# Kernel tuning notes

Measured on AMD Instinct MI355X. Metric: run time of the kernel, lower is better.

## Reference

```python
import jax, jax.numpy as jnp
import numpy as np
from jax import lax

NUM_STATES = 16
NUM_CHAINS = 2
NUM_NODES = 2000
NUM_ITERS = 1000


def setup_inputs() -> dict:
    key = jax.random.key(0)
    k0, k1, k2, k3 = jax.random.split(key, 4)
    return {
        "unnormalized_state_init": jax.random.normal(k0, (NUM_STATES,), dtype=jnp.float32),
        "unnormalized_chain_weights": jax.random.normal(k1, (NUM_STATES, NUM_CHAINS), dtype=jnp.float32),
        "unnormalized_emission_matrix": jax.random.normal(k2, (NUM_STATES, NUM_NODES), dtype=jnp.float32),
        "unnormalized_transition_matrix": jax.random.normal(k3, (NUM_STATES, NUM_STATES), dtype=jnp.float32),
    }


def reference(unnormalized_state_init, unnormalized_chain_weights,
              unnormalized_emission_matrix, unnormalized_transition_matrix):
    # Normalize parameters in log domain (matches torch log_softmax dims)
    log_state_init = jax.nn.log_softmax(unnormalized_state_init, axis=0)            # (S,)
    log_chain_weights = jax.nn.log_softmax(unnormalized_chain_weights, axis=1)      # (S,C)
    log_emission_matrix = jax.nn.log_softmax(unnormalized_emission_matrix, axis=1)  # (S,N)
    log_transition_matrix = jax.nn.log_softmax(unnormalized_transition_matrix, axis=1)  # (S,S)

    # Sequential HMM forward recursion in log domain:
    # h_t[j] = logsumexp_i( h_{t-1}[i] + log_T[i, j] )
    def step(h, _):
        h_next = jax.nn.logsumexp(h[:, None] + log_transition_matrix, axis=0)
        return h_next, h_next

    _, hs = lax.scan(step, log_state_init, None, length=NUM_ITERS - 1)
    log_hidden_state_probs = jnp.concatenate([log_state_init[None, :], hs], axis=0)  # (T,S)

    # P(node | state, chain, iter) joint in log domain: (T,S,C,N)
    # (original repeats emission across the 2 chains; here broadcast over C)
    log_observed_state_probs_ = (
        log_emission_matrix[None, :, None, :]
        + log_chain_weights[None, :, :, None]
        + log_hidden_state_probs[:, :, None, None]
    )
    # Marginalize states then chains (logsumexp over axes 1 then 1 == axes (1,2))
    log_observed_state_probs = jax.nn.logsumexp(log_observed_state_probs_, axis=(1, 2))  # (T,N)
    return log_observed_state_probs
```

## Files before the change

### kernel.cpp

```cpp
#include <hip/hip_runtime.h>
#include <math.h>

#define NN 2000
#define NG 500

__global__ __launch_bounds__(256) void ssm_fused(
    const float* __restrict__ init,
    const float* __restrict__ emis,
    const float* __restrict__ trans,
    float* __restrict__ out)
{
  __shared__ float Tp[16][16];
  __shared__ float Bm[16][16];
  __shared__ float Rm[16][16];
  __shared__ float p0v[16];
  __shared__ float sumExp[16];
  __shared__ float w[4][16];
  __shared__ float wd[4][16];

  const int tid  = threadIdx.x;
  const int i    = tid >> 4, j = tid & 15;
  const int lane = tid & 63, wv = tid >> 6;

  Bm[i][j] = trans[tid];

  float ssum[4] = {0.f, 0.f, 0.f, 0.f};
  for (int g = lane; g < NG; g += 64) {
    #pragma unroll
    for (int si = 0; si < 4; ++si) {
      const int s = wv * 4 + si;
      float4 v = *(const float4*)(emis + s * NN + g * 4);
      ssum[si] += __expf(v.x) + __expf(v.y) + __expf(v.z) + __expf(v.w);
    }
  }
  #pragma unroll
  for (int si = 0; si < 4; ++si) {
    float v = ssum[si];
    #pragma unroll
    for (int off = 32; off > 0; off >>= 1) v += __shfl_down(v, off);
    if (lane == 0) sumExp[wv * 4 + si] = v;
  }

  if (tid < 16) {
    float m = -1e30f, s2 = 0.f;
    #pragma unroll
    for (int k = 0; k < 16; ++k) m = fmaxf(m, init[k]);
    #pragma unroll
    for (int k = 0; k < 16; ++k) s2 += __expf(init[k] - m);
    p0v[tid] = __expf(init[tid] - m) / s2;
  }
  __syncthreads();

  {
    float m = -1e30f;
    #pragma unroll
    for (int k = 0; k < 16; ++k) m = fmaxf(m, Bm[i][k]);
    float sm = 0.f;
    #pragma unroll
    for (int k = 0; k < 16; ++k) sm += __expf(Bm[i][k] - m);
    const float tp = __expf(Bm[i][j] - m) / sm;
    __syncthreads();
    Tp[i][j] = tp;
    Bm[i][j] = tp;
    Rm[i][j] = (i == j) ? 1.f : 0.f;
  }
  __syncthreads();

  #pragma unroll
  for (int q = 0; q < 2; ++q) {
    float acc = 0.f;
    #pragma unroll
    for (int k = 0; k < 16; ++k) acc += Bm[i][k] * Bm[k][j];
    __syncthreads();
    Bm[i][j] = acc;
    __syncthreads();
  }

  int e = blockIdx.x;
  while (e) {
    const bool mul = (e & 1);
    float accR = 0.f, accB = 0.f;
    if (mul) {
      #pragma unroll
      for (int k = 0; k < 16; ++k) accR += Rm[i][k] * Bm[k][j];
    }
    #pragma unroll
    for (int k = 0; k < 16; ++k) accB += Bm[i][k] * Bm[k][j];
    __syncthreads();
    if (mul) Rm[i][j] = accR;
    Bm[i][j] = accB;
    __syncthreads();
    e >>= 1;
  }

  if (tid < 16) {
    float acc = 0.f;
    #pragma unroll
    for (int k = 0; k < 16; ++k) acc += p0v[k] * Rm[k][tid];
    w[0][tid] = acc;
  }
  __syncthreads();
  for (int tt = 1; tt < 4; ++tt) {
    if (tid < 16) {
      float acc = 0.f;
      #pragma unroll
      for (int k = 0; k < 16; ++k) acc += w[tt - 1][k] * Tp[k][tid];
      w[tt][tid] = acc;
    }
    __syncthreads();
  }
  if (tid < 64) wd[tid >> 4][tid & 15] = w[tid >> 4][tid & 15] / sumExp[tid & 15];
  __syncthreads();

  const int tbase = blockIdx.x * 4;
  for (int g = tid; g < NG; g += 256) {
    float4 ex[16];
    #pragma unroll
    for (int s = 0; s < 16; ++s) {
      float4 v = *(const float4*)(emis + s * NN + g * 4);
      ex[s].x = __expf(v.x); ex[s].y = __expf(v.y);
      ex[s].z = __expf(v.z); ex[s].w = __expf(v.w);
    }
    #pragma unroll
    for (int tt = 0; tt < 4; ++tt) {
      float4 acc = make_float4(0.f, 0.f, 0.f, 0.f);
      #pragma unroll
      for (int s = 0; s < 16; ++s) {
        const float p = wd[tt][s];
        acc.x += p * ex[s].x; acc.y += p * ex[s].y;
        acc.z += p * ex[s].z; acc.w += p * ex[s].w;
      }
      float4 o;
      o.x = __logf(acc.x); o.y = __logf(acc.y);
      o.z = __logf(acc.z); o.w = __logf(acc.w);
      *(float4*)(out + (tbase + tt) * NN + g * 4) = o;
    }
  }
}

extern "C" void kernel_launch(void* const* d_in, const int* in_sizes, int n_in,
                              void* d_out, int out_size, void* d_ws, size_t ws_size,
                              hipStream_t stream) {
  const float* init  = (const float*)d_in[0];
  const float* emis  = (const float*)d_in[2];
  const float* trans = (const float*)d_in[3];
  float* out = (float*)d_out;

  hipLaunchKernelGGL(ssm_fused, dim3(250), dim3(256), 0, stream,
                     init, emis, trans, out);
}
```

Measured before the change: 72.92 us.

## Split node columns across a 2D grid and double-buffer matrix powers

The grid becomes 2x250: each block handles 256 of the 500 float4 node groups for its four time steps, where before one block looped over all 500. The matrix-power loop now ping-pongs between two shared buffers, which removes one barrier per squaring. The identity multiply on the first set bit is skipped. Each block still redoes the emission normalisation and matrix exponentiation, so that setup work is duplicated and the second x-block is only partly used.

```diff
diff --git a/kernel.cpp b/kernel.cpp
--- a/kernel.cpp
+++ b/kernel.cpp
@@ -2,7 +2,6 @@
 #include <math.h>
 
 #define NN 2000
-#define NG 500
 
 __global__ __launch_bounds__(256) void ssm_fused(
     const float* __restrict__ init,
@@ -11,21 +10,29 @@
     float* __restrict__ out)
 {
   __shared__ float Tp[16][16];
-  __shared__ float Bm[16][16];
-  __shared__ float Rm[16][16];
+  __shared__ float Bb[2][16][16];
+  __shared__ float Rb[2][16][16];
+  __shared__ float Z[16];
+  __shared__ float wrow[4][16];
   __shared__ float p0v[16];
-  __shared__ float sumExp[16];
-  __shared__ float w[4][16];
-  __shared__ float wd[4][16];
 
   const int tid  = threadIdx.x;
   const int i    = tid >> 4, j = tid & 15;
   const int lane = tid & 63, wv = tid >> 6;
 
-  Bm[i][j] = trans[tid];
+  Rb[0][i][j] = trans[tid];
+
+  if (tid < 16) {
+    float m = -1e30f, s2 = 0.f;
+    #pragma unroll
+    for (int k = 0; k < 16; ++k) m = fmaxf(m, init[k]);
+    #pragma unroll
+    for (int k = 0; k < 16; ++k) s2 += __expf(init[k] - m);
+    p0v[tid] = __expf(init[tid] - m) / s2;
+  }
 
   float ssum[4] = {0.f, 0.f, 0.f, 0.f};
-  for (int g = lane; g < NG; g += 64) {
+  for (int g = lane; g < 500; g += 64) {
     #pragma unroll
     for (int si = 0; si < 4; ++si) {
       const int s = wv * 4 + si;
@@ -38,82 +45,84 @@
     float v = ssum[si];
     #pragma unroll
     for (int off = 32; off > 0; off >>= 1) v += __shfl_down(v, off);
-    if (lane == 0) sumExp[wv * 4 + si] = v;
-  }
-
-  if (tid < 16) {
-    float m = -1e30f, s2 = 0.f;
-    #pragma unroll
-    for (int k = 0; k < 16; ++k) m = fmaxf(m, init[k]);
-    #pragma unroll
-    for (int k = 0; k < 16; ++k) s2 += __expf(init[k] - m);
-    p0v[tid] = __expf(init[tid] - m) / s2;
+    if (lane == 0) Z[wv * 4 + si] = v;
   }
   __syncthreads();
 
   {
     float m = -1e30f;
     #pragma unroll
-    for (int k = 0; k < 16; ++k) m = fmaxf(m, Bm[i][k]);
+    for (int k = 0; k < 16; ++k) m = fmaxf(m, Rb[0][i][k]);
     float sm = 0.f;
     #pragma unroll
-    for (int k = 0; k < 16; ++k) sm += __expf(Bm[i][k] - m);
-    const float tp = __expf(Bm[i][j] - m) / sm;
+    for (int k = 0; k < 16; ++k) sm += __expf(Rb[0][i][k] - m);
+    const float tp = __expf(Rb[0][i][j] - m) / sm;
     __syncthreads();
     Tp[i][j] = tp;
-    Bm[i][j] = tp;
-    Rm[i][j] = (i == j) ? 1.f : 0.f;
+    Bb[0][i][j] = tp;
   }
   __syncthreads();
 
+  int bs = 0;
   #pragma unroll
   for (int q = 0; q < 2; ++q) {
     float acc = 0.f;
     #pragma unroll
-    for (int k = 0; k < 16; ++k) acc += Bm[i][k] * Bm[k][j];
+    for (int k = 0; k < 16; ++k) acc += Bb[bs][i][k] * Bb[bs][k][j];
+    Bb[bs ^ 1][i][j] = acc;
     __syncthreads();
-    Bm[i][j] = acc;
-    __syncthreads();
+    bs ^= 1;
   }
 
-  int e = blockIdx.x;
+  int e = blockIdx.y;
+  int rs = 0;
+  bool rvalid = false;
   while (e) {
     const bool mul = (e & 1);
     float accR = 0.f, accB = 0.f;
     if (mul) {
-      #pragma unroll
-      for (int k = 0; k < 16; ++k) accR += Rm[i][k] * Bm[k][j];
+      if (rvalid) {
+        #pragma unroll
+        for (int k = 0; k < 16; ++k) accR += Rb[rs][i][k] * Bb[bs][k][j];
+      } else {
+        accR = Bb[bs][i][j];
+      }
     }
     #pragma unroll
-    for (int k = 0; k < 16; ++k) accB += Bm[i][k] * Bm[k][j];
+    for (int k = 0; k < 16; ++k) accB += Bb[bs][i][k] * Bb[bs][k][j];
+    if (mul) Rb[rs ^ 1][i][j] = accR;
+    Bb[bs ^ 1][i][j] = accB;
     __syncthreads();
-    if (mul) Rm[i][j] = accR;
-    Bm[i][j] = accB;
-    __syncthreads();
+    if (mul) { rs ^= 1; rvalid = true; }
+    bs ^= 1;
     e >>= 1;
   }
 
   if (tid < 16) {
-    float acc = 0.f;
-    #pragma unroll
-    for (int k = 0; k < 16; ++k) acc += p0v[k] * Rm[k][tid];
-    w[0][tid] = acc;
+    if (rvalid) {
+      float acc = 0.f;
+      #pragma unroll
+      for (int k = 0; k < 16; ++k) acc += p0v[k] * Rb[rs][k][tid];
+      wrow[0][tid] = acc;
+    } else {
+      wrow[0][tid] = p0v[tid];
+    }
   }
   __syncthreads();
   for (int tt = 1; tt < 4; ++tt) {
     if (tid < 16) {
       float acc = 0.f;
       #pragma unroll
-      for (int k = 0; k < 16; ++k) acc += w[tt - 1][k] * Tp[k][tid];
-      w[tt][tid] = acc;
+      for (int k = 0; k < 16; ++k) acc += wrow[tt - 1][k] * Tp[k][tid];
+      wrow[tt][tid] = acc;
     }
     __syncthreads();
   }
-  if (tid < 64) wd[tid >> 4][tid & 15] = w[tid >> 4][tid & 15] / sumExp[tid & 15];
+  if (tid < 64) wrow[tid >> 4][tid & 15] /= Z[tid & 15];
   __syncthreads();
 
-  const int tbase = blockIdx.x * 4;
-  for (int g = tid; g < NG; g += 256) {
+  const int g = blockIdx.x * 256 + tid;
+  if (g < 500) {
     float4 ex[16];
     #pragma unroll
     for (int s = 0; s < 16; ++s) {
@@ -121,12 +130,13 @@
       ex[s].x = __expf(v.x); ex[s].y = __expf(v.y);
       ex[s].z = __expf(v.z); ex[s].w = __expf(v.w);
     }
+    const int tbase = blockIdx.y * 4;
     #pragma unroll
     for (int tt = 0; tt < 4; ++tt) {
       float4 acc = make_float4(0.f, 0.f, 0.f, 0.f);
       #pragma unroll
       for (int s = 0; s < 16; ++s) {
-        const float p = wd[tt][s];
+        const float p = wrow[tt][s];
         acc.x += p * ex[s].x; acc.y += p * ex[s].y;
         acc.z += p * ex[s].z; acc.w += p * ex[s].w;
       }
@@ -146,6 +156,6 @@
   const float* trans = (const float*)d_in[3];
   float* out = (float*)d_out;
 
-  hipLaunchKernelGGL(ssm_fused, dim3(250), dim3(256), 0, stream,
+  hipLaunchKernelGGL(ssm_fused, dim3(2, 250), dim3(256), 0, stream,
                      init, emis, trans, out);
 }
```

New measurement: 72.53 us. No clear change (-0.5%).
